# Kernel tuning notes

Measured on AMD Instinct MI355X. Metric: run time of the kernel, lower is better.

The kernel has to match this reference:

```python
import jax, jax.numpy as jnp
import numpy as np


def setup_inputs() -> dict:
    key = jax.random.key(0)
    k1, k2, k3, k4 = jax.random.split(key, 4)
    B, OUT, IN, K = 64, 4096, 25088, 32
    x = jax.random.normal(k1, (B, IN), dtype=jnp.float32)
    labels = jax.random.randint(k2, (OUT, IN), 0, K, dtype=jnp.int32)
    centroids = jax.random.normal(k3, (K,), dtype=jnp.float32)
    bias = jax.random.normal(k4, (OUT,), dtype=jnp.float32)
    return {"x": x, "labels": labels, "centroids": centroids, "bias": bias}


def reference(x, labels, centroids, bias):
    # Dequantize: reconstruct weight [OUT, IN] by looking labels up in the codebook
    W = centroids[labels]                      # [OUT, IN] gather
    # addmm(bias, x, W.T): [B, IN] @ [IN, OUT] + [OUT]
    return x @ W.T + bias
```

## Files before the change

### kernel.cpp

```cpp
#include <hip/hip_runtime.h>
#include <stdint.h>

typedef float f32x4 __attribute__((ext_vector_type(4)));
typedef short bf16x8 __attribute__((ext_vector_type(8)));

#define IN_DIM   25088
#define OUT_DIM  4096
#define BATCH    64
#define SPLITS   28
#define KBLK     64
#define NBLK     14
#define WG_N     128
#define LSTR     72

__device__ __forceinline__ uint32_t f2bf(float f) {
    uint32_t u = __builtin_bit_cast(uint32_t, f);
    return (u + 0x7FFFu + ((u >> 16) & 1u)) >> 16;
}

__global__ void init_out(const float* __restrict__ bias, float* __restrict__ out) {
    int idx = blockIdx.x * 256 + threadIdx.x;
    out[idx] = bias[idx & (OUT_DIM - 1)];
}

__global__ __launch_bounds__(256) void qlinear_main(
    const float* __restrict__ x,
    const int*   __restrict__ labels,
    const float* __restrict__ centroids,
    float* __restrict__ out)
{
    __shared__ __align__(16) uint32_t table[1024];
    __shared__ __align__(16) uint16_t wt[WG_N * LSTR];
    __shared__ __align__(16) uint16_t xt[BATCH * LSTR];

    const int t = threadIdx.x;
    const int ntiles = OUT_DIM / WG_N;
    const int wgn   = blockIdx.x % ntiles;
    const int split = blockIdx.x / ntiles;
    const int o0    = wgn * WG_N;
    const int kbase = split * (KBLK * NBLK);

    #pragma unroll
    for (int e = 0; e < 4; ++e) {
        int i = t + 256 * e;
        table[i] = f2bf(centroids[i & 31]) | (f2bf(centroids[i >> 5]) << 16);
    }

    f32x4 acc[4][2] = {};

    const int lane = t & 63;
    const int wave = t >> 6;
    const int ln   = lane & 15;
    const int lq   = lane >> 4;

    for (int blk = 0; blk < NBLK; ++blk) {
        const int k0 = kbase + blk * KBLK;
        __syncthreads();

        {
            const int rp  = t >> 4;
            const int kq4 = (t & 15) * 4;
            #pragma unroll
            for (int pass = 0; pass < 8; ++pass) {
                const int row = pass * 16 + rp;
                const int4 lv = *(const int4*)(labels + (size_t)(o0 + row) * IN_DIM + k0 + kq4);
                const uint32_t v01 = table[(uint32_t)lv.x | ((uint32_t)lv.y << 5)];
                const uint32_t v23 = table[(uint32_t)lv.z | ((uint32_t)lv.w << 5)];
                *(uint2*)(wt + row * LSTR + kq4) = make_uint2(v01, v23);
            }
        }
        {
            const int row = t >> 2;
            const int seg = (t & 3) * 16;
            const float* xp = x + (size_t)row * IN_DIM + k0 + seg;
            uint16_t* xw = xt + row * LSTR + seg;
            #pragma unroll
            for (int j = 0; j < 4; ++j) {
                const float4 v = *(const float4*)(xp + j * 4);
                const uint32_t p0 = f2bf(v.x) | (f2bf(v.y) << 16);
                const uint32_t p1 = f2bf(v.z) | (f2bf(v.w) << 16);
                *(uint2*)(xw + j * 4) = make_uint2(p0, p1);
            }
        }
        __syncthreads();

        #pragma unroll
        for (int ks = 0; ks < 2; ++ks) {
            const int kk = ks * 32 + lq * 8;
            bf16x8 a[4], b[2];
            #pragma unroll
            for (int mt = 0; mt < 4; ++mt)
                a[mt] = *(const bf16x8*)(xt + (mt * 16 + ln) * LSTR + kk);
            #pragma unroll
            for (int nt = 0; nt < 2; ++nt)
                b[nt] = *(const bf16x8*)(wt + (wave * 32 + nt * 16 + ln) * LSTR + kk);
            #pragma unroll
            for (int mt = 0; mt < 4; ++mt)
                #pragma unroll
                for (int nt = 0; nt < 2; ++nt)
                    acc[mt][nt] = __builtin_amdgcn_mfma_f32_16x16x32_bf16(
                        a[mt], b[nt], acc[mt][nt], 0, 0, 0);
        }
    }

    #pragma unroll
    for (int mt = 0; mt < 4; ++mt) {
        #pragma unroll
        for (int nt = 0; nt < 2; ++nt) {
            const int o = o0 + wave * 32 + nt * 16 + ln;
            #pragma unroll
            for (int r = 0; r < 4; ++r) {
                const int brow = mt * 16 + lq * 4 + r;
                atomicAdd(out + (size_t)brow * OUT_DIM + o, acc[mt][nt][r]);
            }
        }
    }
}

extern "C" void kernel_launch(void* const* d_in, const int* in_sizes, int n_in,
                              void* d_out, int out_size, void* d_ws, size_t ws_size,
                              hipStream_t stream) {
    const float* x         = (const float*)d_in[0];
    const int*   labels    = (const int*)d_in[1];
    const float* centroids = (const float*)d_in[2];
    const float* bias      = (const float*)d_in[3];
    float* out = (float*)d_out;

    init_out<<<(BATCH * OUT_DIM) / 256, 256, 0, stream>>>(bias, out);
    qlinear_main<<<(OUT_DIM / WG_N) * SPLITS, 256, 0, stream>>>(x, labels, centroids, out);
}
```

Baseline: 564.4 us.

## Pre-convert x to bf16, load A fragments from global, replace atomics with split reduction

Adds a pre-pass that converts x to bf16 once in workspace, so each workgroup no longer re-converts x through LDS for every K block. A-operand MFMA fragments are now loaded straight from global memory into registers and issued before the barrier, which removes the x LDS tile. Label loads are widened to 8 labels per thread. The atomicAdd epilogue is replaced by plain per-split partial stores plus a separate reduce kernel that also adds the bias. This trades atomics for roughly 29 MB of partial-sum traffic and two extra kernel launches.

```diff
diff --git a/kernel.cpp b/kernel.cpp
--- a/kernel.cpp
+++ b/kernel.cpp
@@ -17,80 +17,84 @@
     uint32_t u = __builtin_bit_cast(uint32_t, f);
     return (u + 0x7FFFu + ((u >> 16) & 1u)) >> 16;
 }
+__device__ __forceinline__ uint32_t pack2(float a, float b) {
+    return f2bf(a) | (f2bf(b) << 16);
+}
 
-__global__ void init_out(const float* __restrict__ bias, float* __restrict__ out) {
-    int idx = blockIdx.x * 256 + threadIdx.x;
-    out[idx] = bias[idx & (OUT_DIM - 1)];
+__global__ __launch_bounds__(256) void convert_x(const float* __restrict__ x,
+                                                 uint32_t* __restrict__ xb) {
+    const size_t i = blockIdx.x * 256 + threadIdx.x;
+    const float4 v0 = *(const float4*)(x + i * 8);
+    const float4 v1 = *(const float4*)(x + i * 8 + 4);
+    uint4 o;
+    o.x = pack2(v0.x, v0.y); o.y = pack2(v0.z, v0.w);
+    o.z = pack2(v1.x, v1.y); o.w = pack2(v1.z, v1.w);
+    *(uint4*)(xb + i * 4) = o;
 }
 
 __global__ __launch_bounds__(256) void qlinear_main(
-    const float* __restrict__ x,
-    const int*   __restrict__ labels,
-    const float* __restrict__ centroids,
-    float* __restrict__ out)
+    const int*      __restrict__ labels,
+    const float*    __restrict__ centroids,
+    const uint16_t* __restrict__ xb,
+    float*          __restrict__ part)
 {
     __shared__ __align__(16) uint32_t table[1024];
     __shared__ __align__(16) uint16_t wt[WG_N * LSTR];
-    __shared__ __align__(16) uint16_t xt[BATCH * LSTR];
 
-    const int t = threadIdx.x;
-    const int ntiles = OUT_DIM / WG_N;
-    const int wgn   = blockIdx.x % ntiles;
-    const int split = blockIdx.x / ntiles;
+    const int t     = threadIdx.x;
+    const int wgn   = blockIdx.x & 31;
+    const int split = blockIdx.x >> 5;
     const int o0    = wgn * WG_N;
     const int kbase = split * (KBLK * NBLK);
 
     #pragma unroll
     for (int e = 0; e < 4; ++e) {
-        int i = t + 256 * e;
+        const int i = t + 256 * e;
         table[i] = f2bf(centroids[i & 31]) | (f2bf(centroids[i >> 5]) << 16);
     }
-
-    f32x4 acc[4][2] = {};
 
     const int lane = t & 63;
     const int wave = t >> 6;
     const int ln   = lane & 15;
     const int lq   = lane >> 4;
 
+    const int srow = t >> 3;
+    const int skc  = (t & 7) * 8;
+
+    f32x4 acc[4][2] = {};
+
     for (int blk = 0; blk < NBLK; ++blk) {
         const int k0 = kbase + blk * KBLK;
+
+        bf16x8 a[2][4];
+        #pragma unroll
+        for (int ks = 0; ks < 2; ++ks)
+            #pragma unroll
+            for (int mt = 0; mt < 4; ++mt)
+                a[ks][mt] = *(const bf16x8*)(xb + (size_t)(mt * 16 + ln) * IN_DIM
+                                             + k0 + ks * 32 + lq * 8);
+
         __syncthreads();
 
-        {
-            const int rp  = t >> 4;
-            const int kq4 = (t & 15) * 4;
-            #pragma unroll
-            for (int pass = 0; pass < 8; ++pass) {
-                const int row = pass * 16 + rp;
-                const int4 lv = *(const int4*)(labels + (size_t)(o0 + row) * IN_DIM + k0 + kq4);
-                const uint32_t v01 = table[(uint32_t)lv.x | ((uint32_t)lv.y << 5)];
-                const uint32_t v23 = table[(uint32_t)lv.z | ((uint32_t)lv.w << 5)];
-                *(uint2*)(wt + row * LSTR + kq4) = make_uint2(v01, v23);
-            }
-        }
-        {
-            const int row = t >> 2;
-            const int seg = (t & 3) * 16;
-            const float* xp = x + (size_t)row * IN_DIM + k0 + seg;
-            uint16_t* xw = xt + row * LSTR + seg;
-            #pragma unroll
-            for (int j = 0; j < 4; ++j) {
-                const float4 v = *(const float4*)(xp + j * 4);
-                const uint32_t p0 = f2bf(v.x) | (f2bf(v.y) << 16);
-                const uint32_t p1 = f2bf(v.z) | (f2bf(v.w) << 16);
-                *(uint2*)(xw + j * 4) = make_uint2(p0, p1);
-            }
+        #pragma unroll
+        for (int p = 0; p < 4; ++p) {
+            const int row = p * 32 + srow;
+            const int* lp = labels + (size_t)(o0 + row) * IN_DIM + k0 + skc;
+            const int4 l0 = *(const int4*)lp;
+            const int4 l1 = *(const int4*)(lp + 4);
+            uint4 w;
+            w.x = table[(uint32_t)l0.x | ((uint32_t)l0.y << 5)];
+            w.y = table[(uint32_t)l0.z | ((uint32_t)l0.w << 5)];
+            w.z = table[(uint32_t)l1.x | ((uint32_t)l1.y << 5)];
+            w.w = table[(uint32_t)l1.z | ((uint32_t)l1.w << 5)];
+            *(uint4*)(wt + row * LSTR + skc) = w;
         }
         __syncthreads();
 
         #pragma unroll
         for (int ks = 0; ks < 2; ++ks) {
             const int kk = ks * 32 + lq * 8;
-            bf16x8 a[4], b[2];
-            #pragma unroll
-            for (int mt = 0; mt < 4; ++mt)
-                a[mt] = *(const bf16x8*)(xt + (mt * 16 + ln) * LSTR + kk);
+            bf16x8 b[2];
             #pragma unroll
             for (int nt = 0; nt < 2; ++nt)
                 b[nt] = *(const bf16x8*)(wt + (wave * 32 + nt * 16 + ln) * LSTR + kk);
@@ -99,22 +103,33 @@
                 #pragma unroll
                 for (int nt = 0; nt < 2; ++nt)
                     acc[mt][nt] = __builtin_amdgcn_mfma_f32_16x16x32_bf16(
-                        a[mt], b[nt], acc[mt][nt], 0, 0, 0);
+                        a[ks][mt], b[nt], acc[mt][nt], 0, 0, 0);
         }
     }
 
+    float* pout = part + (size_t)split * (BATCH * OUT_DIM);
     #pragma unroll
-    for (int mt = 0; mt < 4; ++mt) {
+    for (int mt = 0; mt < 4; ++mt)
         #pragma unroll
         for (int nt = 0; nt < 2; ++nt) {
             const int o = o0 + wave * 32 + nt * 16 + ln;
             #pragma unroll
-            for (int r = 0; r < 4; ++r) {
-                const int brow = mt * 16 + lq * 4 + r;
-                atomicAdd(out + (size_t)brow * OUT_DIM + o, acc[mt][nt][r]);
-            }
+            for (int r = 0; r < 4; ++r)
+                pout[(size_t)(mt * 16 + lq * 4 + r) * OUT_DIM + o] = acc[mt][nt][r];
         }
+}
+
+__global__ __launch_bounds__(256) void reduce_out(const float* __restrict__ part,
+                                                  const float* __restrict__ bias,
+                                                  float* __restrict__ out) {
+    const size_t i = blockIdx.x * 256 + threadIdx.x;
+    float4 s = *(const float4*)(bias + ((i * 4) & (OUT_DIM - 1)));
+    #pragma unroll
+    for (int sp = 0; sp < SPLITS; ++sp) {
+        const float4 p = *(const float4*)(part + (size_t)sp * (BATCH * OUT_DIM) + i * 4);
+        s.x += p.x; s.y += p.y; s.z += p.z; s.w += p.w;
     }
+    *(float4*)(out + i * 4) = s;
 }
 
 extern "C" void kernel_launch(void* const* d_in, const int* in_sizes, int n_in,
@@ -126,6 +141,11 @@
     const float* bias      = (const float*)d_in[3];
     float* out = (float*)d_out;
 
-    init_out<<<(BATCH * OUT_DIM) / 256, 256, 0, stream>>>(bias, out);
-    qlinear_main<<<(OUT_DIM / WG_N) * SPLITS, 256, 0, stream>>>(x, labels, centroids, out);
+    uint32_t* xb   = (uint32_t*)d_ws;
+    float*    part = (float*)((char*)d_ws + (size_t)BATCH * IN_DIM * 2);
+
+    convert_x<<<(BATCH * IN_DIM) / 2048, 256, 0, stream>>>(x, xb);
+    qlinear_main<<<32 * SPLITS, 256, 0, stream>>>(labels, centroids,
+                                                  (const uint16_t*)xb, part);
+    reduce_out<<<(BATCH * OUT_DIM) / 1024, 256, 0, stream>>>(part, bias, out);
 }
```

After: 563.6 us. About the same (-0.1%).
